# Kernel optimization log

Hardware: AMD Instinct MI355X
Metric: run time of the kernel (lower is better)

## Reference

```python
import jax, jax.numpy as jnp
import numpy as np

N = 100_000      # nodes
E = 20_000       # hyperedges
NNZ = 1_600_000  # pins (node, hyperedge) pairs
D_IN, D_HID, D_OUT = 128, 128, 64
EPS = 1e-5
NEG_SLOPE = 0.01


def _glorot(key, shape):
    fan_in, fan_out = shape
    lim = np.sqrt(6.0 / (fan_in + fan_out)).astype(np.float32)
    return jax.random.uniform(key, shape, jnp.float32, -lim, lim)


def setup_inputs() -> dict:
    key = jax.random.key(0)
    k = jax.random.split(key, 5)
    x = jax.random.normal(k[0], (N, D_IN), jnp.float32)
    node_idx = jax.random.randint(k[1], (NNZ,), 0, N)
    edge_idx = jax.random.randint(k[2], (NNZ,), 0, E)
    hyperedge_index = jnp.stack([node_idx, edge_idx]).astype(jnp.int64)
    return {
        "x": x,
        "hyperedge_index": hyperedge_index,
        "W1": _glorot(k[3], (D_IN, D_HID)),
        "b1": jnp.zeros((D_HID,), jnp.float32),
        "gamma": jnp.ones((D_HID,), jnp.float32),
        "beta": jnp.zeros((D_HID,), jnp.float32),
        "W3": _glorot(k[4], (D_HID, D_OUT)),
        "b3": jnp.zeros((D_OUT,), jnp.float32),
    }


def hypergraph_conv(x, node_idx, edge_idx, W, b):
    """PyG HypergraphConv (no attention, unit hyperedge weights):
    out = D^-1 H B H^T (x W) + b."""
    x = x @ W  # [N, F]
    ones = jnp.ones(node_idx.shape[0], x.dtype)
    Bdeg = jax.ops.segment_sum(ones, edge_idx, num_segments=E)  # hyperedge degree
    Ddeg = jax.ops.segment_sum(ones, node_idx, num_segments=N)  # node degree
    Binv = jnp.where(Bdeg > 0, 1.0 / Bdeg, 0.0)
    Dinv = jnp.where(Ddeg > 0, 1.0 / Ddeg, 0.0)
    # node -> hyperedge aggregation, scaled by B
    m = jax.ops.segment_sum(x[node_idx], edge_idx, num_segments=E) * Binv[:, None]
    # hyperedge -> node aggregation, scaled by D
    out = jax.ops.segment_sum(m[edge_idx], node_idx, num_segments=N) * Dinv[:, None]
    return out + b


def layer_norm(h, gamma, beta):
    mu = jnp.mean(h, axis=-1, keepdims=True)
    var = jnp.mean(jnp.square(h - mu), axis=-1, keepdims=True)
    return (h - mu) * jax.lax.rsqrt(var + EPS) * gamma + beta


def reference(x, hyperedge_index, W1, b1, gamma, beta, W3, b3):
    node_idx = hyperedge_index[0]
    edge_idx = hyperedge_index[1]
    h = hypergraph_conv(x, node_idx, edge_idx, W1, b1)
    h = layer_norm(h, gamma, beta)
    h = jax.nn.leaky_relu(h, NEG_SLOPE)
    # dropout is identity in eval mode
    z = hypergraph_conv(h, node_idx, edge_idx, W3, b3)
    return z
```

## Files before the change

kernel.cpp:

```cpp
#include <hip/hip_runtime.h>
#include <hip/hip_bf16.h>

#define NNODES 100000
#define NEDGES 20000
#define NPINS  1600000

#define EB_SHIFT 6
#define NB_SHIFT 7
#define NB_E ((NEDGES + 63) / 64)
#define NB_N ((NNODES + 127) / 128)
#define NB_TOT (NB_E + NB_N)
#define ECAP 6144
#define NCAP 2560
#define REG_TOTAL (NB_E * ECAP + NB_N * NCAP)

typedef __attribute__((ext_vector_type(8))) short short8;
typedef __attribute__((ext_vector_type(4))) float f32x4;
typedef unsigned int uint;


static __device__ inline float bf_lo(uint u) { return __uint_as_float(u << 16); }
static __device__ inline float bf_hi(uint u) { return __uint_as_float(u & 0xffff0000u); }

static __device__ inline uint pack_bf2(float a, float b) {
    union { __hip_bfloat16 h; unsigned short u; } ua, ub;
    ua.h = __float2bfloat16(a);
    ub.h = __float2bfloat16(b);
    return ((uint)ub.u << 16) | (uint)ua.u;
}


__global__ void bin_scatter(const int* __restrict__ he, int* __restrict__ ccnt,
                            uint* __restrict__ pairs) {
    __shared__ int hcnt[NB_TOT];
    __shared__ int hbase[NB_TOT];
    int tid = threadIdx.x;
    int base = blockIdx.x * 8192;
    for (int j = tid; j < NB_TOT; j += 256) hcnt[j] = 0;
    __syncthreads();
    for (int k = 0; k < 32; k++) {
        int i = base + k * 256 + tid;
        if (i < NPINS) {
            int n = he[i];
            int e = he[NPINS + i];
            atomicAdd(&hcnt[e >> EB_SHIFT], 1);
            atomicAdd(&hcnt[NB_E + (n >> NB_SHIFT)], 1);
        }
    }
    __syncthreads();
    for (int j = tid; j < NB_TOT; j += 256)
        hbase[j] = hcnt[j] ? atomicAdd(&ccnt[j], hcnt[j]) : 0;
    __syncthreads();
    for (int k = 0; k < 32; k++) {
        int i = base + k * 256 + tid;
        if (i < NPINS) {
            int n = he[i];
            int e = he[NPINS + i];
            int be = e >> EB_SHIFT;
            int pe = atomicAdd(&hbase[be], 1);
            if (pe < ECAP)
                pairs[be * ECAP + pe] = ((uint)(e & 63) << 20) | (uint)n;
            int bn = n >> NB_SHIFT;
            int pn = atomicAdd(&hbase[NB_E + bn], 1);
            if (pn < NCAP)
                pairs[NB_E * ECAP + bn * NCAP + pn] = ((uint)(n & 127) << 20) | (uint)e;
        }
    }
}

template <int KPB, int CAP>
__global__ void bucket_place(const uint* __restrict__ pairs, int regbase,
                             const int* __restrict__ ccnt, int cbase, int kfine_base, int nkeys,
                             int* __restrict__ off, int* __restrict__ cnt,
                             int* __restrict__ pins) {
    constexpr int NIT = CAP / 256;
    __shared__ int fh[KPB];
    __shared__ int fo[KPB];
    __shared__ int fcur[KPB];
    int b = blockIdx.x;
    int tid = threadIdx.x;
    int rb = regbase + b * CAP;
    int count = ccnt[cbase + b];
    if (count > CAP) count = CAP;
    int keyfirst = b * KPB;
    uint pr[NIT];
    for (int k = tid; k < KPB; k += 256) { fh[k] = 0; fcur[k] = 0; }
#pragma unroll
    for (int i = 0; i < NIT; i++) {
        int idx = tid + i * 256;
        if (idx < count) pr[i] = pairs[rb + idx];
    }
    __syncthreads();
#pragma unroll
    for (int i = 0; i < NIT; i++) {
        int idx = tid + i * 256;
        if (idx < count) atomicAdd(&fh[pr[i] >> 20], 1);
    }
    __syncthreads();
    if (tid == 0) {
        int run = rb;
        for (int k = 0; k < KPB; k++) { fo[k] = run; run += fh[k]; }
    }
    __syncthreads();
    for (int k = tid; k < KPB; k += 256) {
        int key = keyfirst + k;
        if (key < nkeys) { off[kfine_base + key] = fo[k]; cnt[kfine_base + key] = fh[k]; }
    }
#pragma unroll
    for (int i = 0; i < NIT; i++) {
        int idx = tid + i * 256;
        if (idx < count) {
            uint p = pr[i];
            int kl = (int)(p >> 20);
            int pos = atomicAdd(&fcur[kl], 1);
            pins[fo[kl] + pos] = (int)(p & 0xFFFFFu);
        }
    }
}


template <int COLS, bool BF16IN>
__global__ void gemm_mfma(const void* __restrict__ Xv, const float* __restrict__ W,
                          unsigned short* __restrict__ Yb) {
    __shared__ __align__(16) char lds[128 * 256 + COLS * 256];
    char* Xl = lds;
    char* Wt = lds + 128 * 256;
    int tid = threadIdx.x;
    long rowbase = (long)blockIdx.x * 128;

    if constexpr (!BF16IN) {
        const float4* X4 = reinterpret_cast<const float4*>(Xv);
#pragma unroll
        for (int i = 0; i < 16; i++) {
            int f = tid + i * 256;
            int r = f >> 5;
            int c4 = f & 31;
            long gr = rowbase + r;
            if (gr > NNODES - 1) gr = NNODES - 1;
            float4 v = X4[gr * 32 + c4];
            uint lo = pack_bf2(v.x, v.y);
            uint hi = pack_bf2(v.z, v.w);
            int byte = r * 256 + ((c4 * 8) ^ ((r & 7) << 4));
            *reinterpret_cast<uint2*>(Xl + byte) = make_uint2(lo, hi);
        }
    } else {
        const uint4* X4 = reinterpret_cast<const uint4*>(Xv);
#pragma unroll
        for (int i = 0; i < 8; i++) {
            int f = tid + i * 256;
            int r = f >> 4;
            int c = f & 15;
            long gr = rowbase + r;
            if (gr > NNODES - 1) gr = NNODES - 1;
            uint4 v = X4[gr * 16 + c];
            int byte = r * 256 + ((c * 16) ^ ((r & 7) << 4));
            *reinterpret_cast<uint4*>(Xl + byte) = v;
        }
    }
    for (int f = tid; f < 128 * COLS / 4; f += 256) {
        int k = f / (COLS / 4);
        int c4 = f % (COLS / 4);
        float4 v = reinterpret_cast<const float4*>(W)[f];
        float vv[4] = {v.x, v.y, v.z, v.w};
#pragma unroll
        for (int j = 0; j < 4; j++) {
            int c = c4 * 4 + j;
            union { __hip_bfloat16 h; short s; } u;
            u.h = __float2bfloat16(vv[j]);
            int byte = c * 256 + ((k * 2) ^ ((c & 7) << 4));
            *reinterpret_cast<short*>(Wt + byte) = u.s;
        }
    }
    __syncthreads();

    constexpr int NF = COLS / 16;
    int wave = tid >> 6;
    int lane = tid & 63;
    int lrow = lane & 15;
    int lq = lane >> 4;
    f32x4 acc[2][NF] = {};

#pragma unroll
    for (int ks = 0; ks < 4; ks++) {
        short8 a[2];
#pragma unroll
        for (int rt = 0; rt < 2; rt++) {
            int r = wave * 32 + rt * 16 + lrow;
            int byte = r * 256 + ((ks * 64 + lq * 16) ^ ((r & 7) << 4));
            a[rt] = *reinterpret_cast<const short8*>(Xl + byte);
        }
#pragma unroll
        for (int nf = 0; nf < NF; nf++) {
            int c = nf * 16 + lrow;
            int byte = c * 256 + ((ks * 64 + lq * 16) ^ ((c & 7) << 4));
            short8 b = *reinterpret_cast<const short8*>(Wt + byte);
            acc[0][nf] = __builtin_amdgcn_mfma_f32_16x16x32_bf16(a[0], b, acc[0][nf], 0, 0, 0);
            acc[1][nf] = __builtin_amdgcn_mfma_f32_16x16x32_bf16(a[1], b, acc[1][nf], 0, 0, 0);
        }
    }

#pragma unroll
    for (int rt = 0; rt < 2; rt++)
#pragma unroll
        for (int nf = 0; nf < NF; nf++)
#pragma unroll
            for (int r = 0; r < 4; r++) {
                long row = rowbase + wave * 32 + rt * 16 + lq * 4 + r;
                if (row < NNODES) {
                    union { __hip_bfloat16 h; unsigned short u; } u;
                    u.h = __float2bfloat16(acc[rt][nf][r]);
                    Yb[row * COLS + nf * 16 + lrow] = u.u;
                }
            }
}


#define ACC_U4(u) do { \
    a0 += bf_lo((u).x); a1 += bf_hi((u).x); a2 += bf_lo((u).y); a3 += bf_hi((u).y); \
    a4 += bf_lo((u).z); a5 += bf_hi((u).z); a6 += bf_lo((u).w); a7 += bf_hi((u).w); } while (0)

#define RED2(x, o1, o2) do { x += __shfl_xor(x, o1); x += __shfl_xor(x, o2); } while (0)
#define REDQ(o1, o2) do { RED2(a0,o1,o2); RED2(a1,o1,o2); RED2(a2,o1,o2); RED2(a3,o1,o2); \
                          RED2(a4,o1,o2); RED2(a5,o1,o2); RED2(a6,o1,o2); RED2(a7,o1,o2); } while (0)

__global__ void edge_agg_128(const uint4* __restrict__ feat4, const int* __restrict__ pins,
                             const int* __restrict__ off, const int* __restrict__ cnt,
                             uint4* __restrict__ outp) {
    int s = blockIdx.x * 4 + (threadIdx.x >> 6);
    if (s >= NEDGES) return;
    int lane = threadIdx.x & 63;
    int q = lane >> 4, fp = lane & 15;
    int start = off[s], c = cnt[s];
    float a0 = 0.f, a1 = 0.f, a2 = 0.f, a3 = 0.f, a4 = 0.f, a5 = 0.f, a6 = 0.f, a7 = 0.f;
    for (int cb = 0; cb < c; cb += 64) {
        int rem = c - cb;
        int lim = rem < 64 ? rem : 64;
        int pk = 0;
        if (lane < lim) pk = pins[start + cb + lane];
        int i = 0;
        for (; i + 16 <= lim; i += 16) {
            int pa = __shfl(pk, i + q);
            int pb = __shfl(pk, i + 4 + q);
            int pc = __shfl(pk, i + 8 + q);
            int pd = __shfl(pk, i + 12 + q);
            uint4 ua = feat4[(uint)pa * 16 + fp];
            uint4 ub = feat4[(uint)pb * 16 + fp];
            uint4 uc = feat4[(uint)pc * 16 + fp];
            uint4 ud = feat4[(uint)pd * 16 + fp];
            ACC_U4(ua); ACC_U4(ub); ACC_U4(uc); ACC_U4(ud);
        }
        for (; i + 4 <= lim; i += 4) {
            int p = __shfl(pk, i + q);
            uint4 u = feat4[(uint)p * 16 + fp];
            ACC_U4(u);
        }
        if (i < lim) {
            int idx = i + q;
            int p = __shfl(pk, idx < lim ? idx : i);
            if (idx < lim) {
                uint4 u = feat4[(uint)p * 16 + fp];
                ACC_U4(u);
            }
        }
    }
    REDQ(16, 32);
    if (q == 0) {
        float inv = (c > 0) ? (1.f / (float)c) : 0.f;
        outp[(uint)s * 16 + fp] = make_uint4(pack_bf2(a0 * inv, a1 * inv),
                                             pack_bf2(a2 * inv, a3 * inv),
                                             pack_bf2(a4 * inv, a5 * inv),
                                             pack_bf2(a6 * inv, a7 * inv));
    }
}

__global__ void node_agg_ln(const uint4* __restrict__ m4, const int* __restrict__ pins,
                            const int* __restrict__ off, const int* __restrict__ cnt,
                            const float* __restrict__ b1, const float* __restrict__ gamma,
                            const float* __restrict__ beta, uint4* __restrict__ hout) {
    int s = blockIdx.x * 4 + (threadIdx.x >> 6);
    if (s >= NNODES) return;
    int lane = threadIdx.x & 63;
    int q = lane >> 4, fp = lane & 15;
    int start = off[s], c = cnt[s];
    float a0 = 0.f, a1 = 0.f, a2 = 0.f, a3 = 0.f, a4 = 0.f, a5 = 0.f, a6 = 0.f, a7 = 0.f;
    for (int cb = 0; cb < c; cb += 64) {
        int rem = c - cb;
        int lim = rem < 64 ? rem : 64;
        int pk = 0;
        if (lane < lim) pk = pins[start + cb + lane];
        int i = 0;
        for (; i + 16 <= lim; i += 16) {
            int pa = __shfl(pk, i + q);
            int pb = __shfl(pk, i + 4 + q);
            int pc = __shfl(pk, i + 8 + q);
            int pd = __shfl(pk, i + 12 + q);
            uint4 ua = m4[(uint)pa * 16 + fp];
            uint4 ub = m4[(uint)pb * 16 + fp];
            uint4 uc = m4[(uint)pc * 16 + fp];
            uint4 ud = m4[(uint)pd * 16 + fp];
            ACC_U4(ua); ACC_U4(ub); ACC_U4(uc); ACC_U4(ud);
        }
        for (; i + 4 <= lim; i += 4) {
            int p = __shfl(pk, i + q);
            uint4 u = m4[(uint)p * 16 + fp];
            ACC_U4(u);
        }
        if (i < lim) {
            int idx = i + q;
            int p = __shfl(pk, idx < lim ? idx : i);
            if (idx < lim) {
                uint4 u = m4[(uint)p * 16 + fp];
                ACC_U4(u);
            }
        }
    }
    REDQ(16, 32);
    float dinv = (c > 0) ? (1.f / (float)c) : 0.f;
    float4 bb0 = reinterpret_cast<const float4*>(b1)[fp * 2];
    float4 bb1 = reinterpret_cast<const float4*>(b1)[fp * 2 + 1];
    float v0 = a0 * dinv + bb0.x;
    float v1 = a1 * dinv + bb0.y;
    float v2 = a2 * dinv + bb0.z;
    float v3 = a3 * dinv + bb0.w;
    float v4 = a4 * dinv + bb1.x;
    float v5 = a5 * dinv + bb1.y;
    float v6 = a6 * dinv + bb1.z;
    float v7 = a7 * dinv + bb1.w;
    float sum = ((v0 + v1) + (v2 + v3)) + ((v4 + v5) + (v6 + v7));
    float sq = ((v0 * v0 + v1 * v1) + (v2 * v2 + v3 * v3)) +
               ((v4 * v4 + v5 * v5) + (v6 * v6 + v7 * v7));
#pragma unroll
    for (int o = 1; o < 16; o <<= 1) {
        sum += __shfl_xor(sum, o);
        sq  += __shfl_xor(sq, o);
    }
    float mu = sum * (1.f / 128.f);
    float var = sq * (1.f / 128.f) - mu * mu;
    float rstd = rsqrtf(var + 1e-5f);
    if (q == 0) {
        float4 g0  = reinterpret_cast<const float4*>(gamma)[fp * 2];
        float4 g1  = reinterpret_cast<const float4*>(gamma)[fp * 2 + 1];
        float4 be0 = reinterpret_cast<const float4*>(beta)[fp * 2];
        float4 be1 = reinterpret_cast<const float4*>(beta)[fp * 2 + 1];
        float h0 = (v0 - mu) * rstd * g0.x + be0.x;
        float h1 = (v1 - mu) * rstd * g0.y + be0.y;
        float h2 = (v2 - mu) * rstd * g0.z + be0.z;
        float h3 = (v3 - mu) * rstd * g0.w + be0.w;
        float h4 = (v4 - mu) * rstd * g1.x + be1.x;
        float h5 = (v5 - mu) * rstd * g1.y + be1.y;
        float h6 = (v6 - mu) * rstd * g1.z + be1.z;
        float h7 = (v7 - mu) * rstd * g1.w + be1.w;
        h0 = (h0 > 0.f) ? h0 : 0.01f * h0;
        h1 = (h1 > 0.f) ? h1 : 0.01f * h1;
        h2 = (h2 > 0.f) ? h2 : 0.01f * h2;
        h3 = (h3 > 0.f) ? h3 : 0.01f * h3;
        h4 = (h4 > 0.f) ? h4 : 0.01f * h4;
        h5 = (h5 > 0.f) ? h5 : 0.01f * h5;
        h6 = (h6 > 0.f) ? h6 : 0.01f * h6;
        h7 = (h7 > 0.f) ? h7 : 0.01f * h7;
        hout[(uint)s * 16 + fp] = make_uint4(pack_bf2(h0, h1), pack_bf2(h2, h3),
                                             pack_bf2(h4, h5), pack_bf2(h6, h7));
    }
}

#define REDE(o1, o2, o3) do { \
    a0 += __shfl_xor(a0, o1); a0 += __shfl_xor(a0, o2); a0 += __shfl_xor(a0, o3); \
    a1 += __shfl_xor(a1, o1); a1 += __shfl_xor(a1, o2); a1 += __shfl_xor(a1, o3); \
    a2 += __shfl_xor(a2, o1); a2 += __shfl_xor(a2, o2); a2 += __shfl_xor(a2, o3); \
    a3 += __shfl_xor(a3, o1); a3 += __shfl_xor(a3, o2); a3 += __shfl_xor(a3, o3); \
    a4 += __shfl_xor(a4, o1); a4 += __shfl_xor(a4, o2); a4 += __shfl_xor(a4, o3); \
    a5 += __shfl_xor(a5, o1); a5 += __shfl_xor(a5, o2); a5 += __shfl_xor(a5, o3); \
    a6 += __shfl_xor(a6, o1); a6 += __shfl_xor(a6, o2); a6 += __shfl_xor(a6, o3); \
    a7 += __shfl_xor(a7, o1); a7 += __shfl_xor(a7, o2); a7 += __shfl_xor(a7, o3); } while (0)

__global__ void edge_agg_64(const uint4* __restrict__ feat4, const int* __restrict__ pins,
                            const int* __restrict__ off, const int* __restrict__ cnt,
                            uint4* __restrict__ outp) {
    int s = blockIdx.x * 4 + (threadIdx.x >> 6);
    if (s >= NEDGES) return;
    int lane = threadIdx.x & 63;
    int e = lane >> 3, fp = lane & 7;
    int start = off[s], c = cnt[s];
    float a0 = 0.f, a1 = 0.f, a2 = 0.f, a3 = 0.f, a4 = 0.f, a5 = 0.f, a6 = 0.f, a7 = 0.f;
    for (int cb = 0; cb < c; cb += 64) {
        int rem = c - cb;
        int lim = rem < 64 ? rem : 64;
        int pk = 0;
        if (lane < lim) pk = pins[start + cb + lane];
        int i = 0;
        for (; i + 32 <= lim; i += 32) {
            int pa = __shfl(pk, i + e);
            int pb = __shfl(pk, i + 8 + e);
            int pc = __shfl(pk, i + 16 + e);
            int pd = __shfl(pk, i + 24 + e);
            uint4 ua = feat4[(uint)pa * 8 + fp];
            uint4 ub = feat4[(uint)pb * 8 + fp];
            uint4 uc = feat4[(uint)pc * 8 + fp];
            uint4 ud = feat4[(uint)pd * 8 + fp];
            ACC_U4(ua); ACC_U4(ub); ACC_U4(uc); ACC_U4(ud);
        }
        for (; i + 8 <= lim; i += 8) {
            int p = __shfl(pk, i + e);
            uint4 u = feat4[(uint)p * 8 + fp];
            ACC_U4(u);
        }
        if (i < lim) {
            int idx = i + e;
            int p = __shfl(pk, idx < lim ? idx : i);
            if (idx < lim) {
                uint4 u = feat4[(uint)p * 8 + fp];
                ACC_U4(u);
            }
        }
    }
    REDE(8, 16, 32);
    if (e == 0) {
        float inv = (c > 0) ? (1.f / (float)c) : 0.f;
        outp[(uint)s * 8 + fp] = make_uint4(pack_bf2(a0 * inv, a1 * inv),
                                            pack_bf2(a2 * inv, a3 * inv),
                                            pack_bf2(a4 * inv, a5 * inv),
                                            pack_bf2(a6 * inv, a7 * inv));
    }
}

__global__ void node_agg_out(const uint4* __restrict__ m4, const int* __restrict__ pins,
                             const int* __restrict__ off, const int* __restrict__ cnt,
                             const float* __restrict__ b3, float4* __restrict__ out4) {
    int s = blockIdx.x * 4 + (threadIdx.x >> 6);
    if (s >= NNODES) return;
    int lane = threadIdx.x & 63;
    int e = lane >> 3, fp = lane & 7;
    int start = off[s], c = cnt[s];
    float a0 = 0.f, a1 = 0.f, a2 = 0.f, a3 = 0.f, a4 = 0.f, a5 = 0.f, a6 = 0.f, a7 = 0.f;
    for (int cb = 0; cb < c; cb += 64) {
        int rem = c - cb;
        int lim = rem < 64 ? rem : 64;
        int pk = 0;
        if (lane < lim) pk = pins[start + cb + lane];
        int i = 0;
        for (; i + 32 <= lim; i += 32) {
            int pa = __shfl(pk, i + e);
            int pb = __shfl(pk, i + 8 + e);
            int pc = __shfl(pk, i + 16 + e);
            int pd = __shfl(pk, i + 24 + e);
            uint4 ua = m4[(uint)pa * 8 + fp];
            uint4 ub = m4[(uint)pb * 8 + fp];
            uint4 uc = m4[(uint)pc * 8 + fp];
            uint4 ud = m4[(uint)pd * 8 + fp];
            ACC_U4(ua); ACC_U4(ub); ACC_U4(uc); ACC_U4(ud);
        }
        for (; i + 8 <= lim; i += 8) {
            int p = __shfl(pk, i + e);
            uint4 u = m4[(uint)p * 8 + fp];
            ACC_U4(u);
        }
        if (i < lim) {
            int idx = i + e;
            int p = __shfl(pk, idx < lim ? idx : i);
            if (idx < lim) {
                uint4 u = m4[(uint)p * 8 + fp];
                ACC_U4(u);
            }
        }
    }
    REDE(8, 16, 32);
    if (e == 0) {
        float inv = (c > 0) ? (1.f / (float)c) : 0.f;
        float4 bb0 = reinterpret_cast<const float4*>(b3)[fp * 2];
        float4 bb1 = reinterpret_cast<const float4*>(b3)[fp * 2 + 1];
        out4[(uint)s * 16 + fp * 2] = make_float4(a0 * inv + bb0.x, a1 * inv + bb0.y,
                                                  a2 * inv + bb0.z, a3 * inv + bb0.w);
        out4[(uint)s * 16 + fp * 2 + 1] = make_float4(a4 * inv + bb1.x, a5 * inv + bb1.y,
                                                      a6 * inv + bb1.z, a7 * inv + bb1.w);
    }
}


extern "C" void kernel_launch(void* const* d_in, const int* in_sizes, int n_in,
                              void* d_out, int out_size, void* d_ws, size_t ws_size,
                              hipStream_t stream) {
    const float* x     = (const float*)d_in[0];
    const int*   he    = (const int*)d_in[1];
    const float* W1    = (const float*)d_in[2];
    const float* b1    = (const float*)d_in[3];
    const float* gamma = (const float*)d_in[4];
    const float* beta  = (const float*)d_in[5];
    const float* W3    = (const float*)d_in[6];
    const float* b3    = (const float*)d_in[7];
    float* out = (float*)d_out;

    char* ws = (char*)d_ws;
    uint* xWb = (uint*)ws;
    uint* mb  = (uint*)(ws + 25600000);
    uint* hb  = (uint*)(ws + 25600000 + 5120000);
    char* ip  = ws + 25600000 + 5120000 + 25600000;
    int* off  = (int*)ip;
    int* cnt  = off + (NEDGES + NNODES);
    int* ccnt = cnt + (NEDGES + NNODES);
    int* pins = ccnt + NB_TOT + 64;
    uint* pairs = (uint*)ws;

    const int nblkA = (NPINS + 8191) / 8192;
    const int ngemm = (NNODES + 127) / 128;

    hipMemsetAsync(ccnt, 0, sizeof(int) * NB_TOT, stream);
    bin_scatter<<<nblkA, 256, 0, stream>>>(he, ccnt, pairs);
    bucket_place<64, ECAP><<<NB_E, 256, 0, stream>>>(pairs, 0, ccnt, 0, 0, NEDGES,
                                                     off, cnt, pins);
    bucket_place<128, NCAP><<<NB_N, 256, 0, stream>>>(pairs, NB_E * ECAP, ccnt, NB_E,
                                                      NEDGES, NNODES, off, cnt, pins);

    gemm_mfma<128, false><<<ngemm, 256, 0, stream>>>(x, W1, (unsigned short*)xWb);
    edge_agg_128<<<(NEDGES + 3) / 4, 256, 0, stream>>>((const uint4*)xWb, pins, off, cnt,
                                                       (uint4*)mb);
    node_agg_ln<<<(NNODES + 3) / 4, 256, 0, stream>>>((const uint4*)mb, pins, off + NEDGES,
                                                      cnt + NEDGES, b1, gamma, beta,
                                                      (uint4*)hb);
    gemm_mfma<64, true><<<ngemm, 256, 0, stream>>>(hb, W3, (unsigned short*)xWb);
    edge_agg_64<<<(NEDGES + 3) / 4, 256, 0, stream>>>((const uint4*)xWb, pins, off, cnt,
                                                      (uint4*)mb);
    node_agg_out<<<(NNODES + 3) / 4, 256, 0, stream>>>((const uint4*)mb, pins, off + NEDGES,
                                                       cnt + NEDGES, b3, (float4*)out);
}
```

Baseline: 291.0 us.

## Merge first GEMM with pin binning and fuse both bucket-place passes

New measurement: 276.8 us. -4.9%, faster.

```diff
diff --git a/kernel.cpp b/kernel.cpp
--- a/kernel.cpp
+++ b/kernel.cpp
@@ -30,12 +30,108 @@
 }
 
 
-__global__ void bin_scatter(const int* __restrict__ he, int* __restrict__ ccnt,
-                            uint* __restrict__ pairs) {
-    __shared__ int hcnt[NB_TOT];
-    __shared__ int hbase[NB_TOT];
+template <int COLS, bool BF16IN>
+static __device__ __forceinline__ void gemm_body(const void* __restrict__ Xv,
+                                                 const float* __restrict__ W,
+                                                 unsigned short* __restrict__ Yb,
+                                                 long rowbase, char* lds) {
+    char* Xl = lds;
+    char* Wt = lds + 128 * 256;
     int tid = threadIdx.x;
-    int base = blockIdx.x * 8192;
+
+    if constexpr (!BF16IN) {
+        const float4* X4 = reinterpret_cast<const float4*>(Xv);
+#pragma unroll
+        for (int i = 0; i < 16; i++) {
+            int f = tid + i * 256;
+            int r = f >> 5;
+            int c4 = f & 31;
+            long gr = rowbase + r;
+            if (gr > NNODES - 1) gr = NNODES - 1;
+            float4 v = X4[gr * 32 + c4];
+            uint lo = pack_bf2(v.x, v.y);
+            uint hi = pack_bf2(v.z, v.w);
+            int byte = r * 256 + ((c4 * 8) ^ ((r & 7) << 4));
+            *reinterpret_cast<uint2*>(Xl + byte) = make_uint2(lo, hi);
+        }
+    } else {
+        const uint4* X4 = reinterpret_cast<const uint4*>(Xv);
+#pragma unroll
+        for (int i = 0; i < 8; i++) {
+            int f = tid + i * 256;
+            int r = f >> 4;
+            int c = f & 15;
+            long gr = rowbase + r;
+            if (gr > NNODES - 1) gr = NNODES - 1;
+            uint4 v = X4[gr * 16 + c];
+            int byte = r * 256 + ((c * 16) ^ ((r & 7) << 4));
+            *reinterpret_cast<uint4*>(Xl + byte) = v;
+        }
+    }
+    for (int f = tid; f < 128 * COLS / 4; f += 256) {
+        int k = f / (COLS / 4);
+        int c4 = f % (COLS / 4);
+        float4 v = reinterpret_cast<const float4*>(W)[f];
+        float vv[4] = {v.x, v.y, v.z, v.w};
+#pragma unroll
+        for (int j = 0; j < 4; j++) {
+            int c = c4 * 4 + j;
+            union { __hip_bfloat16 h; short s; } u;
+            u.h = __float2bfloat16(vv[j]);
+            int byte = c * 256 + ((k * 2) ^ ((c & 7) << 4));
+            *reinterpret_cast<short*>(Wt + byte) = u.s;
+        }
+    }
+    __syncthreads();
+
+    constexpr int NF = COLS / 16;
+    int wave = tid >> 6;
+    int lane = tid & 63;
+    int lrow = lane & 15;
+    int lq = lane >> 4;
+    f32x4 acc[2][NF] = {};
+
+#pragma unroll
+    for (int ks = 0; ks < 4; ks++) {
+        short8 a[2];
+#pragma unroll
+        for (int rt = 0; rt < 2; rt++) {
+            int r = wave * 32 + rt * 16 + lrow;
+            int byte = r * 256 + ((ks * 64 + lq * 16) ^ ((r & 7) << 4));
+            a[rt] = *reinterpret_cast<const short8*>(Xl + byte);
+        }
+#pragma unroll
+        for (int nf = 0; nf < NF; nf++) {
+            int c = nf * 16 + lrow;
+            int byte = c * 256 + ((ks * 64 + lq * 16) ^ ((c & 7) << 4));
+            short8 b = *reinterpret_cast<const short8*>(Wt + byte);
+            acc[0][nf] = __builtin_amdgcn_mfma_f32_16x16x32_bf16(a[0], b, acc[0][nf], 0, 0, 0);
+            acc[1][nf] = __builtin_amdgcn_mfma_f32_16x16x32_bf16(a[1], b, acc[1][nf], 0, 0, 0);
+        }
+    }
+
+#pragma unroll
+    for (int rt = 0; rt < 2; rt++)
+#pragma unroll
+        for (int nf = 0; nf < NF; nf++)
+#pragma unroll
+            for (int r = 0; r < 4; r++) {
+                long row = rowbase + wave * 32 + rt * 16 + lq * 4 + r;
+                if (row < NNODES) {
+                    union { __hip_bfloat16 h; unsigned short u; } u;
+                    u.h = __float2bfloat16(acc[rt][nf][r]);
+                    Yb[row * COLS + nf * 16 + lrow] = u.u;
+                }
+            }
+}
+
+
+static __device__ __forceinline__ void scatter_body(const int* __restrict__ he,
+                                                    int* __restrict__ ccnt,
+                                                    uint* __restrict__ pairs,
+                                                    int sb, int* hcnt, int* hbase) {
+    int tid = threadIdx.x;
+    int base = sb * 8192;
     for (int j = tid; j < NB_TOT; j += 256) hcnt[j] = 0;
     __syncthreads();
     for (int k = 0; k < 32; k++) {
@@ -68,16 +164,36 @@
     }
 }
 
+__global__ void k1_gemm_scatter(const float* __restrict__ x, const float* __restrict__ W1,
+                                unsigned short* __restrict__ xWb, const int* __restrict__ he,
+                                int* __restrict__ ccnt, uint* __restrict__ pairs) {
+    __shared__ __align__(16) char lds[128 * 256 + 128 * 256];
+    int b = blockIdx.x;
+    if (b % 5 == 4) {
+        int* hcnt = (int*)lds;
+        scatter_body(he, ccnt, pairs, b / 5, hcnt, hcnt + NB_TOT);
+    } else {
+        int g = b - (b + 1) / 5;
+        if (g < (NNODES + 127) / 128)
+            gemm_body<128, false>(x, W1, xWb, (long)g * 128, lds);
+    }
+}
+
+__global__ void gemm2_kernel(const void* __restrict__ Xv, const float* __restrict__ W,
+                             unsigned short* __restrict__ Yb) {
+    __shared__ __align__(16) char lds[128 * 256 + 64 * 256];
+    gemm_body<64, true>(Xv, W, Yb, (long)blockIdx.x * 128, lds);
+}
+
+
 template <int KPB, int CAP>
-__global__ void bucket_place(const uint* __restrict__ pairs, int regbase,
-                             const int* __restrict__ ccnt, int cbase, int kfine_base, int nkeys,
-                             int* __restrict__ off, int* __restrict__ cnt,
-                             int* __restrict__ pins) {
+static __device__ __forceinline__ void place_body(const uint* __restrict__ pairs, int regbase,
+                                                  const int* __restrict__ ccnt, int cbase,
+                                                  int kfine_base, int nkeys,
+                                                  int* __restrict__ off, int* __restrict__ cnt,
+                                                  int* __restrict__ pins, int b,
+                                                  int* fh, int* fo, int* fcur) {
     constexpr int NIT = CAP / 256;
-    __shared__ int fh[KPB];
-    __shared__ int fo[KPB];
-    __shared__ int fcur[KPB];
-    int b = blockIdx.x;
     int tid = threadIdx.x;
     int rb = regbase + b * CAP;
     int count = ccnt[cbase + b];
@@ -118,100 +234,16 @@
     }
 }
 
-
-template <int COLS, bool BF16IN>
-__global__ void gemm_mfma(const void* __restrict__ Xv, const float* __restrict__ W,
-                          unsigned short* __restrict__ Yb) {
-    __shared__ __align__(16) char lds[128 * 256 + COLS * 256];
-    char* Xl = lds;
-    char* Wt = lds + 128 * 256;
-    int tid = threadIdx.x;
-    long rowbase = (long)blockIdx.x * 128;
-
-    if constexpr (!BF16IN) {
-        const float4* X4 = reinterpret_cast<const float4*>(Xv);
-#pragma unroll
-        for (int i = 0; i < 16; i++) {
-            int f = tid + i * 256;
-            int r = f >> 5;
-            int c4 = f & 31;
-            long gr = rowbase + r;
-            if (gr > NNODES - 1) gr = NNODES - 1;
-            float4 v = X4[gr * 32 + c4];
-            uint lo = pack_bf2(v.x, v.y);
-            uint hi = pack_bf2(v.z, v.w);
-            int byte = r * 256 + ((c4 * 8) ^ ((r & 7) << 4));
-            *reinterpret_cast<uint2*>(Xl + byte) = make_uint2(lo, hi);
-        }
-    } else {
-        const uint4* X4 = reinterpret_cast<const uint4*>(Xv);
-#pragma unroll
-        for (int i = 0; i < 8; i++) {
-            int f = tid + i * 256;
-            int r = f >> 4;
-            int c = f & 15;
-            long gr = rowbase + r;
-            if (gr > NNODES - 1) gr = NNODES - 1;
-            uint4 v = X4[gr * 16 + c];
-            int byte = r * 256 + ((c * 16) ^ ((r & 7) << 4));
-            *reinterpret_cast<uint4*>(Xl + byte) = v;
-        }
-    }
-    for (int f = tid; f < 128 * COLS / 4; f += 256) {
-        int k = f / (COLS / 4);
-        int c4 = f % (COLS / 4);
-        float4 v = reinterpret_cast<const float4*>(W)[f];
-        float vv[4] = {v.x, v.y, v.z, v.w};
-#pragma unroll
-        for (int j = 0; j < 4; j++) {
-            int c = c4 * 4 + j;
-            union { __hip_bfloat16 h; short s; } u;
-            u.h = __float2bfloat16(vv[j]);
-            int byte = c * 256 + ((k * 2) ^ ((c & 7) << 4));
-            *reinterpret_cast<short*>(Wt + byte) = u.s;
-        }
-    }
-    __syncthreads();
-
-    constexpr int NF = COLS / 16;
-    int wave = tid >> 6;
-    int lane = tid & 63;
-    int lrow = lane & 15;
-    int lq = lane >> 4;
-    f32x4 acc[2][NF] = {};
-
-#pragma unroll
-    for (int ks = 0; ks < 4; ks++) {
-        short8 a[2];
-#pragma unroll
-        for (int rt = 0; rt < 2; rt++) {
-            int r = wave * 32 + rt * 16 + lrow;
-            int byte = r * 256 + ((ks * 64 + lq * 16) ^ ((r & 7) << 4));
-            a[rt] = *reinterpret_cast<const short8*>(Xl + byte);
-        }
-#pragma unroll
-        for (int nf = 0; nf < NF; nf++) {
-            int c = nf * 16 + lrow;
-            int byte = c * 256 + ((ks * 64 + lq * 16) ^ ((c & 7) << 4));
-            short8 b = *reinterpret_cast<const short8*>(Wt + byte);
-            acc[0][nf] = __builtin_amdgcn_mfma_f32_16x16x32_bf16(a[0], b, acc[0][nf], 0, 0, 0);
-            acc[1][nf] = __builtin_amdgcn_mfma_f32_16x16x32_bf16(a[1], b, acc[1][nf], 0, 0, 0);
-        }
-    }
-
-#pragma unroll
-    for (int rt = 0; rt < 2; rt++)
-#pragma unroll
-        for (int nf = 0; nf < NF; nf++)
-#pragma unroll
-            for (int r = 0; r < 4; r++) {
-                long row = rowbase + wave * 32 + rt * 16 + lq * 4 + r;
-                if (row < NNODES) {
-                    union { __hip_bfloat16 h; unsigned short u; } u;
-                    u.h = __float2bfloat16(acc[rt][nf][r]);
-                    Yb[row * COLS + nf * 16 + lrow] = u.u;
-                }
-            }
+__global__ void k2_place(const uint* __restrict__ pairs, const int* __restrict__ ccnt,
+                         int* __restrict__ off, int* __restrict__ cnt,
+                         int* __restrict__ pins) {
+    __shared__ int fh[128], fo[128], fcur[128];
+    int b = blockIdx.x;
+    if (b < NB_E)
+        place_body<64, ECAP>(pairs, 0, ccnt, 0, 0, NEDGES, off, cnt, pins, b, fh, fo, fcur);
+    else
+        place_body<128, NCAP>(pairs, NB_E * ECAP, ccnt, NB_E, NEDGES, NNODES, off, cnt, pins,
+                              b - NB_E, fh, fo, fcur);
 }
 
 
@@ -492,31 +524,24 @@
     char* ws = (char*)d_ws;
     uint* xWb = (uint*)ws;
     uint* mb  = (uint*)(ws + 25600000);
-    uint* hb  = (uint*)(ws + 25600000 + 5120000);
-    char* ip  = ws + 25600000 + 5120000 + 25600000;
+    uint* hb  = (uint*)(ws + 30720000);
+    char* ip  = ws + 56320000;
     int* off  = (int*)ip;
     int* cnt  = off + (NEDGES + NNODES);
     int* ccnt = cnt + (NEDGES + NNODES);
     int* pins = ccnt + NB_TOT + 64;
-    uint* pairs = (uint*)ws;
-
-    const int nblkA = (NPINS + 8191) / 8192;
-    const int ngemm = (NNODES + 127) / 128;
+    uint* pairs = (uint*)(ws + 73400000);
 
     hipMemsetAsync(ccnt, 0, sizeof(int) * NB_TOT, stream);
-    bin_scatter<<<nblkA, 256, 0, stream>>>(he, ccnt, pairs);
-    bucket_place<64, ECAP><<<NB_E, 256, 0, stream>>>(pairs, 0, ccnt, 0, 0, NEDGES,
-                                                     off, cnt, pins);
-    bucket_place<128, NCAP><<<NB_N, 256, 0, stream>>>(pairs, NB_E * ECAP, ccnt, NB_E,
-                                                      NEDGES, NNODES, off, cnt, pins);
-
-    gemm_mfma<128, false><<<ngemm, 256, 0, stream>>>(x, W1, (unsigned short*)xWb);
+    k1_gemm_scatter<<<980, 256, 0, stream>>>(x, W1, (unsigned short*)xWb, he, ccnt, pairs);
+    k2_place<<<NB_TOT, 256, 0, stream>>>(pairs, ccnt, off, cnt, pins);
+
     edge_agg_128<<<(NEDGES + 3) / 4, 256, 0, stream>>>((const uint4*)xWb, pins, off, cnt,
                                                        (uint4*)mb);
     node_agg_ln<<<(NNODES + 3) / 4, 256, 0, stream>>>((const uint4*)mb, pins, off + NEDGES,
                                                       cnt + NEDGES, b1, gamma, beta,
                                                       (uint4*)hb);
-    gemm_mfma<64, true><<<ngemm, 256, 0, stream>>>(hb, W3, (unsigned short*)xWb);
+    gemm2_kernel<<<(NNODES + 127) / 128, 256, 0, stream>>>(hb, W3, (unsigned short*)xWb);
     edge_agg_64<<<(NEDGES + 3) / 4, 256, 0, stream>>>((const uint4*)xWb, pins, off, cnt,
                                                       (uint4*)mb);
     node_agg_out<<<(NNODES + 3) / 4, 256, 0, stream>>>((const uint4*)mb, pins, off + NEDGES,
```
